# Performance work log

Hardware: AMD Instinct MI355X
Metric: run time of the kernel (lower is better)

## Reference

```python
import jax, jax.numpy as jnp
import numpy as np

E = 384        # number of edges
HID = 128      # hidden_dim
NH = 8         # num_heads
DH = HID // NH # head_dim = 16
NR = 64        # num_radial
CUTOFF = 10.0
AIN = 2 * DH + NR + 1  # attention MLP input dim = 97


def _xavier(key, fan_in, fan_out):
    a = np.sqrt(6.0 / (fan_in + fan_out))
    return jax.random.uniform(key, (fan_in, fan_out), jnp.float32, -a, a)


def setup_inputs() -> dict:
    key = jax.random.key(0)
    ks = jax.random.split(key, 16)
    return {
        "edge_features": jax.random.normal(ks[0], (E, HID), jnp.float32),
        "edge_coords": jax.random.normal(ks[1], (E, 3), jnp.float32),
        "edge_mask": jnp.zeros((E, E), jnp.float32),  # 0 = connected
        "wq": _xavier(ks[2], HID, HID),
        "wk": _xavier(ks[3], HID, HID),
        "wv": _xavier(ks[4], HID, HID),
        "rbf_centers": jnp.linspace(0.0, CUTOFF, NR).astype(jnp.float32),
        "rbf_widths": jnp.full((NR,), 0.5, jnp.float32),
        "a_w1": _xavier(ks[5], AIN, HID), "a_b1": jnp.zeros((HID,), jnp.float32),
        "a_w2": _xavier(ks[6], HID, HID), "a_b2": jnp.zeros((HID,), jnp.float32),
        "a_w3": _xavier(ks[7], HID, NH),  "a_b3": jnp.zeros((NH,), jnp.float32),
        "g_w1": _xavier(ks[8], DH, HID),  "g_b1": jnp.zeros((HID,), jnp.float32),
        "g_w2": _xavier(ks[9], HID, 1),   "g_b2": jnp.zeros((1,), jnp.float32),
        "wo": _xavier(ks[10], HID, HID),  "bo": jnp.zeros((HID,), jnp.float32),
        "ln_g": jnp.ones((HID,), jnp.float32),
        "ln_b": jnp.zeros((HID,), jnp.float32),
        "edge_index": jax.random.randint(ks[11], (2, E), 0, E, jnp.int64) if jax.config.jax_enable_x64 else jax.random.randint(ks[11], (2, E), 0, E, jnp.int32),
    }


def reference(edge_features, edge_coords, edge_mask,
              wq, wk, wv, rbf_centers, rbf_widths,
              a_w1, a_b1, a_w2, a_b2, a_w3, a_b3,
              g_w1, g_b1, g_w2, g_b2, wo, bo, ln_g, ln_b,
              edge_index):
    silu = jax.nn.silu
    n = edge_features.shape[0]

    q = (edge_features @ wq).reshape(n, NH, DH)
    k = (edge_features @ wk).reshape(n, NH, DH)
    v = (edge_features @ wv).reshape(n, NH, DH)

    # pairwise geometry [E, E, ...]
    coord_diff = edge_coords[:, None, :] - edge_coords[None, :, :]
    dist = jnp.linalg.norm(coord_diff, axis=-1) + 1e-8
    dist = jnp.clip(dist, 1e-8, 1e8)
    dot = jnp.clip(jnp.sum(edge_coords[:, None, :] * edge_coords[None, :, :], -1),
                   -1e8, 1e8)
    d = dist[..., None]                               # [E, E, 1]
    rbf = jnp.exp(-rbf_widths * (d - rbf_centers) ** 2) * (d <= CUTOFF).astype(jnp.float32)

    feats = []
    coords = edge_coords
    for h in range(NH):  # structural loop over fixed num_heads
        qh = jnp.broadcast_to(q[:, h, None, :], (n, n, DH))
        kh = jnp.broadcast_to(k[None, :, h, :], (n, n, DH))
        ai = jnp.concatenate([qh, kh, rbf, dot[..., None]], -1)  # [E, E, 97]
        x = silu(ai @ a_w1 + a_b1)
        x = silu(x @ a_w2 + a_b2)
        scores = (x @ a_w3 + a_b3)[:, :, h] + edge_mask
        scores = jnp.clip(scores, -1e9, 1e9)
        attn = jax.nn.softmax(scores, axis=-1)
        attn = jnp.nan_to_num(attn, nan=0.0, posinf=1.0, neginf=0.0)
        vh = v[:, h, :]
        feats.append(attn @ vh)
        # coord gate from v_head of the query edge, broadcast over keys
        gates = jax.nn.sigmoid(silu(vh @ g_w1 + g_b1) @ g_w2 + g_b2)  # [E, 1]
        coords = coords + jnp.einsum('ij,ijc->ic', attn * gates, coord_diff) / NH

    upd = jnp.concatenate(feats, -1)             # [E, hidden]
    y = edge_features + upd @ wo + bo            # residual + out_proj
    mu = jnp.mean(y, -1, keepdims=True)
    var = jnp.var(y, -1, keepdims=True)
    out_f = (y - mu) / jnp.sqrt(var + 1e-5) * ln_g + ln_b
    return out_f, coords
```

## Files before the change

### kernel.cpp

```cpp
#include <hip/hip_runtime.h>
#include <hip/hip_bf16.h>

#define N 384
#define HIDN 128
#define NHD 8
#define DHD 16
#define NRB 64
#define CUTF 10.0f

#define WS_V 0
#define WS_QPB (WS_V + N*HIDN)
#define WS_KPB (WS_QPB + N*NHD*HIDN/2)
#define WS_GATE (WS_KPB + N*NHD*HIDN/2)
#define WS_UPD (WS_GATE + N*NHD)
#define WS_SCORES (WS_UPD + N*HIDN)
#define WS_W2BF (WS_SCORES + NHD*N*N)

typedef short bf16x8 __attribute__((ext_vector_type(8)));
typedef float floatx4 __attribute__((ext_vector_type(4)));
#define MFMA16(a, b, c) __builtin_amdgcn_mfma_f32_16x16x32_bf16(a, b, c, 0, 0, 0)

__device__ __forceinline__ float siluf(float x) { return x / (1.0f + __expf(-x)); }
__device__ __forceinline__ float silu_fast(float x) {
    return x * __builtin_amdgcn_rcpf(1.0f + __expf(-x));
}
__device__ __forceinline__ short f2bf(float f) {
    unsigned int b = __float_as_uint(f);
    unsigned int r = (b + 0x7fffu + ((b >> 16) & 1u)) >> 16;
    return (short)r;
}
__device__ __forceinline__ float bf2f(short s) {
    return __uint_as_float(((unsigned int)(unsigned short)s) << 16);
}
__device__ __forceinline__ unsigned int cvt_pk_bf16(float lo, float hi) {
    unsigned int r;
    asm("v_cvt_pk_bf16_f32 %0, %1, %2" : "=v"(r) : "v"(lo), "v"(hi));
    return r;
}
__device__ __forceinline__ float wave_sum(float v) {
    for (int o = 32; o; o >>= 1) v += __shfl_down(v, o, 64);
    return v;
}

__global__ __launch_bounds__(128) void k_pre(const float* __restrict__ ef,
    const float* __restrict__ wq, const float* __restrict__ wk, const float* __restrict__ wv,
    const float* __restrict__ aw1, const float* __restrict__ aw2,
    const float* __restrict__ gw1, const float* __restrict__ gb1,
    const float* __restrict__ gw2, const float* __restrict__ gb2,
    float* __restrict__ v, unsigned short* __restrict__ Qpb,
    unsigned short* __restrict__ Kpb, float* __restrict__ gates,
    unsigned short* __restrict__ w2bf) {
    __shared__ float sE[HIDN], sQ[HIDN], sK[HIDN], sV[HIDN];
    __shared__ float sRed[2];
    int i = blockIdx.x, t = threadIdx.x;
    if (i < HIDN) w2bf[(size_t)i * HIDN + t] = (unsigned short)f2bf(aw2[t * HIDN + i]);
    sE[t] = ef[i * HIDN + t];
    __syncthreads();
    float aq = 0.f, ak = 0.f, av = 0.f;
#pragma unroll 8
    for (int c = 0; c < HIDN; c++) {
        float e = sE[c];
        aq += e * wq[c * HIDN + t];
        ak += e * wk[c * HIDN + t];
        av += e * wv[c * HIDN + t];
    }
    v[i * HIDN + t] = av;
    sQ[t] = aq; sK[t] = ak; sV[t] = av;
    __syncthreads();
    for (int h = 0; h < NHD; h++) {
        float accq = 0.f, acck = 0.f;
#pragma unroll
        for (int d = 0; d < DHD; d++) {
            accq += sQ[h * DHD + d] * aw1[d * HIDN + t];
            acck += sK[h * DHD + d] * aw1[(DHD + d) * HIDN + t];
        }
        Qpb[(i * NHD + h) * HIDN + t] = (unsigned short)f2bf(accq);
        Kpb[(i * NHD + h) * HIDN + t] = (unsigned short)f2bf(acck);
        float tt = gb1[t];
#pragma unroll
        for (int d = 0; d < DHD; d++) tt += sV[h * DHD + d] * gw1[d * HIDN + t];
        float contrib = siluf(tt) * gw2[t];
        float s = wave_sum(contrib);
        if ((t & 63) == 0) sRed[t >> 6] = s;
        __syncthreads();
        if (t == 0) gates[i * NHD + h] = 1.0f / (1.0f + __expf(-(sRed[0] + sRed[1] + gb2[0])));
        __syncthreads();
    }
}

#define OFF_W2T 0
#define OFF_QPB 32768
#define OFF_SDD 34816
#define OFF_RBF 34944
#define OFF_R   39040
#define SMEM_SZ 55936

__global__ __launch_bounds__(512, 4) void k_scores_mfma(
    const float* __restrict__ coords, const float* __restrict__ mask,
    const float* __restrict__ centers, const float* __restrict__ widths,
    const float* __restrict__ aw1, const float* __restrict__ ab1,
    const float* __restrict__ ab2,
    const float* __restrict__ aw3, const float* __restrict__ ab3,
    const unsigned short* __restrict__ Qpb, const unsigned short* __restrict__ Kpb,
    const unsigned short* __restrict__ w2bf,
    float* __restrict__ scores) {
    __shared__ __align__(16) char smem[SMEM_SZ];
    const int t = threadIdx.x;
    const int lane = t & 63;
    const int w = t >> 6;
    const int l15 = lane & 15;
    const int quad = lane >> 4;
    const int i = blockIdx.y;
    const int jb = blockIdx.x * 128;

    {
        const uint4* src = (const uint4*)w2bf;
        for (int idx = t; idx < 2048; idx += 512) {
            int row = idx >> 4, slot = idx & 15;
            *(uint4*)(smem + OFF_W2T + row * 256 + ((slot * 16) ^ ((row & 7) << 4))) = src[idx];
        }
    }
    if (t < 128) {
        ((uint4*)(smem + OFF_QPB))[t] = ((const uint4*)(Qpb + (size_t)i * NHD * HIDN))[t];
    }
    const int c0 = w * 16 + l15;
    bf16x8 BW1[2];
#pragma unroll
    for (int ks = 0; ks < 2; ks++) {
        bf16x8 a;
#pragma unroll
        for (int e = 0; e < 8; e++) {
            int r = ks * 32 + quad * 8 + e;
            a[e] = f2bf(aw1[(32 + r) * HIDN + c0]);
        }
        BW1[ks] = a;
    }
    const float b1v = ab1[c0];
    const float w1dv = aw1[96 * HIDN + c0];
    const float ab3v = ab3[w];
    float b2r[8], w3r[8];
#pragma unroll
    for (int ct = 0; ct < 8; ct++) {
        b2r[ct] = ab2[ct * 16 + l15];
        w3r[ct] = aw3[(ct * 16 + l15) * NHD + w];
    }
    const float cr = centers[t & 63], rwd = widths[t & 63];
    const float cix = coords[i * 3], ciy = coords[i * 3 + 1], ciz = coords[i * 3 + 2];
    __syncthreads();

    for (int ch = 0; ch < 4; ch++) {
        const int j0 = jb + ch * 32;
        {
            int r = t & 63;
#pragma unroll
            for (int p = 0; p < 4; p++) {
                int j = w + p * 8;
                int jj = j0 + j;
                float jx = coords[jj * 3], jy = coords[jj * 3 + 1], jz = coords[jj * 3 + 2];
                float dx = cix - jx, dy = ciy - jy, dz = ciz - jz;
                float dist = sqrtf(dx * dx + dy * dy + dz * dz) + 1e-8f;
                dist = fminf(fmaxf(dist, 1e-8f), 1e8f);
                float dd = dist - cr;
                float val = (dist <= CUTF) ? __expf(-rwd * dd * dd) : 0.0f;
                *(short*)(smem + OFF_RBF + j * 128 + ((r * 2) ^ ((j & 7) << 4))) = f2bf(val);
            }
            if (t < 32) {
                int jj = j0 + t;
                float jx = coords[jj * 3], jy = coords[jj * 3 + 1], jz = coords[jj * 3 + 2];
                float dot = fminf(fmaxf(cix * jx + ciy * jy + ciz * jz, -1e8f), 1e8f);
                *(float*)(smem + OFF_SDD + t * 4) = dot;
            }
        }
        __syncthreads();
#pragma unroll
        for (int jt = 0; jt < 2; jt++) {
            int jl = jt * 16 + l15;
            int sw = (jl & 7) << 4;
            bf16x8 ra0 = *(const bf16x8*)(smem + OFF_RBF + jl * 128 + ((quad * 16) ^ sw));
            bf16x8 ra1 = *(const bf16x8*)(smem + OFF_RBF + jl * 128 + ((64 + quad * 16) ^ sw));
            floatx4 acc;
#pragma unroll
            for (int r = 0; r < 4; r++) {
                float dotv = *(const float*)(smem + OFF_SDD + (jt * 16 + quad * 4 + r) * 4);
                acc[r] = b1v + dotv * w1dv;
            }
            acc = MFMA16(ra0, BW1[0], acc);
            acc = MFMA16(ra1, BW1[1], acc);
#pragma unroll
            for (int r = 0; r < 4; r++)
                *(float*)(smem + OFF_R + (jt * 16 + quad * 4 + r) * 528 + c0 * 4) = acc[r];
        }
        __syncthreads();
        {
            bf16x8 A2[2][4];
#pragma unroll
            for (int f = 0; f < 4; f++) {
                const int c8 = f * 32 + quad * 8;
                bf16x8 qp = *(const bf16x8*)(smem + OFF_QPB + (w * HIDN + c8) * 2);
#pragma unroll
                for (int jt = 0; jt < 2; jt++) {
                    const int jl = jt * 16 + l15;
                    bf16x8 kp = *(const bf16x8*)(Kpb + ((size_t)(j0 + jl) * NHD + w) * HIDN + c8);
                    const char* rbase = smem + OFF_R + jl * 528 + c8 * 4;
                    float4 r0 = *(const float4*)(rbase);
                    float4 r1 = *(const float4*)(rbase + 16);
                    float xs[8] = {r0.x, r0.y, r0.z, r0.w, r1.x, r1.y, r1.z, r1.w};
                    union { unsigned int u[4]; bf16x8 v; } uu;
#pragma unroll
                    for (int e2 = 0; e2 < 4; e2++) {
                        float xa = silu_fast(bf2f(kp[2 * e2])     + bf2f(qp[2 * e2])     + xs[2 * e2]);
                        float xb = silu_fast(bf2f(kp[2 * e2 + 1]) + bf2f(qp[2 * e2 + 1]) + xs[2 * e2 + 1]);
                        uu.u[e2] = cvt_pk_bf16(xa, xb);
                    }
                    A2[jt][f] = uu.v;
                }
            }
            float part0[4] = {0.f, 0.f, 0.f, 0.f};
            float part1[4] = {0.f, 0.f, 0.f, 0.f};
#pragma unroll 2
            for (int ct = 0; ct < 8; ct++) {
                const int rw2 = ct * 16 + l15;
                const char* wb = smem + OFF_W2T + rw2 * 256;
                const int sw = (rw2 & 7) << 4;
                bf16x8 b0 = *(const bf16x8*)(wb + ((quad * 16) ^ sw));
                bf16x8 b1 = *(const bf16x8*)(wb + ((64 + quad * 16) ^ sw));
                bf16x8 b2 = *(const bf16x8*)(wb + ((128 + quad * 16) ^ sw));
                bf16x8 b3 = *(const bf16x8*)(wb + ((192 + quad * 16) ^ sw));
                float bb = b2r[ct], ww = w3r[ct];
                floatx4 acc0 = {bb, bb, bb, bb};
                acc0 = MFMA16(A2[0][0], b0, acc0);
                acc0 = MFMA16(A2[0][1], b1, acc0);
                acc0 = MFMA16(A2[0][2], b2, acc0);
                acc0 = MFMA16(A2[0][3], b3, acc0);
                floatx4 acc1 = {bb, bb, bb, bb};
                acc1 = MFMA16(A2[1][0], b0, acc1);
                acc1 = MFMA16(A2[1][1], b1, acc1);
                acc1 = MFMA16(A2[1][2], b2, acc1);
                acc1 = MFMA16(A2[1][3], b3, acc1);
#pragma unroll
                for (int r = 0; r < 4; r++) {
                    part0[r] += silu_fast(acc0[r]) * ww;
                    part1[r] += silu_fast(acc1[r]) * ww;
                }
            }
#pragma unroll
            for (int off = 1; off < 16; off <<= 1) {
#pragma unroll
                for (int r = 0; r < 4; r++) {
                    part0[r] += __shfl_xor(part0[r], off, 64);
                    part1[r] += __shfl_xor(part1[r], off, 64);
                }
            }
            if (l15 == 0) {
#pragma unroll
                for (int r = 0; r < 4; r++) {
                    int j = quad * 4 + r;
                    float s = part0[r] + ab3v + mask[(size_t)i * N + j0 + j];
                    s = fminf(fmaxf(s, -1e9f), 1e9f);
                    scores[((size_t)w * N + i) * N + j0 + j] = s;
                    int j2 = 16 + quad * 4 + r;
                    float s2 = part1[r] + ab3v + mask[(size_t)i * N + j0 + j2];
                    s2 = fminf(fmaxf(s2, -1e9f), 1e9f);
                    scores[((size_t)w * N + i) * N + j0 + j2] = s2;
                }
            }
        }
        __syncthreads();
    }
}

__global__ __launch_bounds__(256) void k_attn2(
    const float* __restrict__ scores, const float* __restrict__ v,
    const float* __restrict__ gates, const float* __restrict__ coords,
    float* __restrict__ upd, float* __restrict__ out) {
    __shared__ float sA[4][N];
    __shared__ float sCrd[N * 3];
    __shared__ float sC[NHD][3];
    int i = blockIdx.x, t = threadIdx.x, w = t >> 6, lane = t & 63;
    for (int idx = t; idx < N * 3; idx += 256) sCrd[idx] = coords[idx];
    float cix = coords[i * 3], ciy = coords[i * 3 + 1], ciz = coords[i * 3 + 2];
    __syncthreads();
    for (int hh = 0; hh < 2; hh++) {
        int h = hh * 4 + w;
        const float* srow = scores + ((size_t)h * N + i) * N;
        float s[6];
#pragma unroll
        for (int p = 0; p < 6; p++) s[p] = srow[lane + 64 * p];
        float m = s[0];
#pragma unroll
        for (int p = 1; p < 6; p++) m = fmaxf(m, s[p]);
        for (int off = 1; off < 64; off <<= 1) m = fmaxf(m, __shfl_xor(m, off, 64));
        float e[6], sum = 0.f;
#pragma unroll
        for (int p = 0; p < 6; p++) { e[p] = __expf(s[p] - m); sum += e[p]; }
        for (int off = 1; off < 64; off <<= 1) sum += __shfl_xor(sum, off, 64);
        float inv = 1.0f / sum;
#pragma unroll
        for (int p = 0; p < 6; p++) sA[w][lane + 64 * p] = e[p] * inv;
        __syncthreads();
        int d4 = lane & 3, grp = lane >> 2;
        float4 f4 = {0.f, 0.f, 0.f, 0.f};
        for (int j = grp; j < N; j += 16) {
            float a = sA[w][j];
            float4 vv = *(const float4*)(v + j * HIDN + h * DHD + d4 * 4);
            f4.x += a * vv.x; f4.y += a * vv.y; f4.z += a * vv.z; f4.w += a * vv.w;
        }
#pragma unroll
        for (int off = 4; off < 64; off <<= 1) {
            f4.x += __shfl_xor(f4.x, off, 64);
            f4.y += __shfl_xor(f4.y, off, 64);
            f4.z += __shfl_xor(f4.z, off, 64);
            f4.w += __shfl_xor(f4.w, off, 64);
        }
        if (lane < 4) *(float4*)(upd + i * HIDN + h * DHD + lane * 4) = f4;
        float cx = 0.f, cy = 0.f, cz = 0.f;
#pragma unroll
        for (int p = 0; p < 6; p++) {
            int j = lane + 64 * p;
            float a = sA[w][j];
            cx += a * (cix - sCrd[j * 3]);
            cy += a * (ciy - sCrd[j * 3 + 1]);
            cz += a * (ciz - sCrd[j * 3 + 2]);
        }
        for (int off = 1; off < 64; off <<= 1) {
            cx += __shfl_xor(cx, off, 64);
            cy += __shfl_xor(cy, off, 64);
            cz += __shfl_xor(cz, off, 64);
        }
        if (lane == 0) {
            float g = gates[i * NHD + h] * (1.0f / NHD);
            sC[h][0] = g * cx; sC[h][1] = g * cy; sC[h][2] = g * cz;
        }
        __syncthreads();
    }
    if (t < 3) {
        float acc = coords[i * 3 + t];
#pragma unroll
        for (int h = 0; h < NHD; h++) acc += sC[h][t];
        out[N * HIDN + i * 3 + t] = acc;
    }
}

__global__ __launch_bounds__(128) void k_out(
    const float* __restrict__ ef, const float* __restrict__ upd,
    const float* __restrict__ wo, const float* __restrict__ bo,
    const float* __restrict__ lng, const float* __restrict__ lnb,
    float* __restrict__ out) {
    __shared__ float sU[HIDN];
    __shared__ float sR[2];
    int i = blockIdx.x, c = threadIdx.x;
    sU[c] = upd[i * HIDN + c];
    __syncthreads();
    float y = ef[i * HIDN + c] + bo[c];
#pragma unroll 8
    for (int cp = 0; cp < HIDN; cp++) y += sU[cp] * wo[cp * HIDN + c];
    float s = wave_sum(y);
    if ((c & 63) == 0) sR[c >> 6] = s;
    __syncthreads();
    float mu = (sR[0] + sR[1]) * (1.0f / HIDN);
    __syncthreads();
    float dv = y - mu;
    float s2 = wave_sum(dv * dv);
    if ((c & 63) == 0) sR[c >> 6] = s2;
    __syncthreads();
    float var = (sR[0] + sR[1]) * (1.0f / HIDN);
    out[i * HIDN + c] = dv * rsqrtf(var + 1e-5f) * lng[c] + lnb[c];
}

extern "C" void kernel_launch(void* const* d_in, const int* in_sizes, int n_in,
                              void* d_out, int out_size, void* d_ws, size_t ws_size,
                              hipStream_t stream) {
    const float* ef      = (const float*)d_in[0];
    const float* coords  = (const float*)d_in[1];
    const float* mask    = (const float*)d_in[2];
    const float* wq      = (const float*)d_in[3];
    const float* wk      = (const float*)d_in[4];
    const float* wv      = (const float*)d_in[5];
    const float* centers = (const float*)d_in[6];
    const float* widths  = (const float*)d_in[7];
    const float* aw1     = (const float*)d_in[8];
    const float* ab1     = (const float*)d_in[9];
    const float* aw2     = (const float*)d_in[10];
    const float* ab2     = (const float*)d_in[11];
    const float* aw3     = (const float*)d_in[12];
    const float* ab3     = (const float*)d_in[13];
    const float* gw1     = (const float*)d_in[14];
    const float* gb1     = (const float*)d_in[15];
    const float* gw2     = (const float*)d_in[16];
    const float* gb2     = (const float*)d_in[17];
    const float* wo      = (const float*)d_in[18];
    const float* bo      = (const float*)d_in[19];
    const float* lng     = (const float*)d_in[20];
    const float* lnb     = (const float*)d_in[21];
    float* ws = (float*)d_ws;
    float* v      = ws + WS_V;
    unsigned short* Qpb = (unsigned short*)(ws + WS_QPB);
    unsigned short* Kpb = (unsigned short*)(ws + WS_KPB);
    float* gates  = ws + WS_GATE;
    float* upd    = ws + WS_UPD;
    float* scores = ws + WS_SCORES;
    unsigned short* w2bf = (unsigned short*)(ws + WS_W2BF);
    float* out = (float*)d_out;

    k_pre<<<N, 128, 0, stream>>>(ef, wq, wk, wv, aw1, aw2, gw1, gb1, gw2, gb2, v, Qpb, Kpb, gates, w2bf);
    k_scores_mfma<<<dim3(3, N), 512, 0, stream>>>(
        coords, mask, centers, widths, aw1, ab1, ab2, aw3, ab3, Qpb, Kpb, w2bf, scores);
    k_attn2<<<N, 256, 0, stream>>>(scores, v, gates, coords, upd, out);
    k_out<<<N, 128, 0, stream>>>(ef, upd, wo, bo, lng, lnb, out);
}
```

Baseline: 277.8 us.

## Fuse output projection into attention kernel and retile score kernel

Merges the out-projection and layernorm kernel into the attention kernel, dropping one launch and the upd round trip through global memory. Reorganizes the score kernel: half the j range per block (doubling grid size), head-major Q/K projection layout, Q loaded into registers instead of shared memory, one j-tile processed at a time to cut register pressure, higher occupancy hint, and vectorized mask/score stores. Gate reductions in the prologue kernel are batched behind one barrier instead of two per head. Smaller blocks reload W2 into shared memory twice as often, which is the main cost added.

```diff
diff --git a/kernel.cpp b/kernel.cpp
--- a/kernel.cpp
+++ b/kernel.cpp
@@ -51,7 +51,7 @@
     unsigned short* __restrict__ Kpb, float* __restrict__ gates,
     unsigned short* __restrict__ w2bf) {
     __shared__ float sE[HIDN], sQ[HIDN], sK[HIDN], sV[HIDN];
-    __shared__ float sRed[2];
+    __shared__ float sG[NHD][2];
     int i = blockIdx.x, t = threadIdx.x;
     if (i < HIDN) w2bf[(size_t)i * HIDN + t] = (unsigned short)f2bf(aw2[t * HIDN + i]);
     sE[t] = ef[i * HIDN + t];
@@ -74,28 +74,27 @@
             accq += sQ[h * DHD + d] * aw1[d * HIDN + t];
             acck += sK[h * DHD + d] * aw1[(DHD + d) * HIDN + t];
         }
-        Qpb[(i * NHD + h) * HIDN + t] = (unsigned short)f2bf(accq);
-        Kpb[(i * NHD + h) * HIDN + t] = (unsigned short)f2bf(acck);
+        Qpb[((size_t)h * N + i) * HIDN + t] = (unsigned short)f2bf(accq);
+        Kpb[((size_t)h * N + i) * HIDN + t] = (unsigned short)f2bf(acck);
         float tt = gb1[t];
 #pragma unroll
         for (int d = 0; d < DHD; d++) tt += sV[h * DHD + d] * gw1[d * HIDN + t];
         float contrib = siluf(tt) * gw2[t];
         float s = wave_sum(contrib);
-        if ((t & 63) == 0) sRed[t >> 6] = s;
-        __syncthreads();
-        if (t == 0) gates[i * NHD + h] = 1.0f / (1.0f + __expf(-(sRed[0] + sRed[1] + gb2[0])));
-        __syncthreads();
-    }
+        if ((t & 63) == 0) sG[h][t >> 6] = s;
+    }
+    __syncthreads();
+    if (t < NHD)
+        gates[i * NHD + t] = 1.0f / (1.0f + __expf(-(sG[t][0] + sG[t][1] + gb2[0])));
 }
 
 #define OFF_W2T 0
-#define OFF_QPB 32768
-#define OFF_SDD 34816
-#define OFF_RBF 34944
-#define OFF_R   39040
-#define SMEM_SZ 55936
-
-__global__ __launch_bounds__(512, 4) void k_scores_mfma(
+#define OFF_SDD 32768
+#define OFF_RBF 32896
+#define OFF_R   36992
+#define SMEM_SZ 53888
+
+__global__ __launch_bounds__(512, 6) void k_scores_mfma(
     const float* __restrict__ coords, const float* __restrict__ mask,
     const float* __restrict__ centers, const float* __restrict__ widths,
     const float* __restrict__ aw1, const float* __restrict__ ab1,
@@ -111,7 +110,7 @@
     const int l15 = lane & 15;
     const int quad = lane >> 4;
     const int i = blockIdx.y;
-    const int jb = blockIdx.x * 128;
+    const int jb = blockIdx.x * 64;
 
     {
         const uint4* src = (const uint4*)w2bf;
@@ -120,9 +119,6 @@
             *(uint4*)(smem + OFF_W2T + row * 256 + ((slot * 16) ^ ((row & 7) << 4))) = src[idx];
         }
     }
-    if (t < 128) {
-        ((uint4*)(smem + OFF_QPB))[t] = ((const uint4*)(Qpb + (size_t)i * NHD * HIDN))[t];
-    }
     const int c0 = w * 16 + l15;
     bf16x8 BW1[2];
 #pragma unroll
@@ -135,6 +131,10 @@
         }
         BW1[ks] = a;
     }
+    bf16x8 QPF[4];
+#pragma unroll
+    for (int f = 0; f < 4; f++)
+        QPF[f] = *(const bf16x8*)(Qpb + ((size_t)w * N + i) * HIDN + f * 32 + quad * 8);
     const float b1v = ab1[c0];
     const float w1dv = aw1[96 * HIDN + c0];
     const float ab3v = ab3[w];
@@ -144,14 +144,13 @@
         b2r[ct] = ab2[ct * 16 + l15];
         w3r[ct] = aw3[(ct * 16 + l15) * NHD + w];
     }
-    const float cr = centers[t & 63], rwd = widths[t & 63];
+    const float cr = centers[lane], rwd = widths[lane];
     const float cix = coords[i * 3], ciy = coords[i * 3 + 1], ciz = coords[i * 3 + 2];
     __syncthreads();
 
-    for (int ch = 0; ch < 4; ch++) {
+    for (int ch = 0; ch < 2; ch++) {
         const int j0 = jb + ch * 32;
         {
-            int r = t & 63;
 #pragma unroll
             for (int p = 0; p < 4; p++) {
                 int j = w + p * 8;
@@ -162,7 +161,7 @@
                 dist = fminf(fmaxf(dist, 1e-8f), 1e8f);
                 float dd = dist - cr;
                 float val = (dist <= CUTF) ? __expf(-rwd * dd * dd) : 0.0f;
-                *(short*)(smem + OFF_RBF + j * 128 + ((r * 2) ^ ((j & 7) << 4))) = f2bf(val);
+                *(short*)(smem + OFF_RBF + j * 128 + ((lane * 2) ^ ((j & 7) << 4))) = f2bf(val);
             }
             if (t < 32) {
                 int jj = j0 + t;
@@ -191,32 +190,29 @@
                 *(float*)(smem + OFF_R + (jt * 16 + quad * 4 + r) * 528 + c0 * 4) = acc[r];
         }
         __syncthreads();
-        {
-            bf16x8 A2[2][4];
+#pragma unroll
+        for (int jt = 0; jt < 2; jt++) {
+            const int jl = jt * 16 + l15;
+            bf16x8 A[4];
 #pragma unroll
             for (int f = 0; f < 4; f++) {
                 const int c8 = f * 32 + quad * 8;
-                bf16x8 qp = *(const bf16x8*)(smem + OFF_QPB + (w * HIDN + c8) * 2);
-#pragma unroll
-                for (int jt = 0; jt < 2; jt++) {
-                    const int jl = jt * 16 + l15;
-                    bf16x8 kp = *(const bf16x8*)(Kpb + ((size_t)(j0 + jl) * NHD + w) * HIDN + c8);
-                    const char* rbase = smem + OFF_R + jl * 528 + c8 * 4;
-                    float4 r0 = *(const float4*)(rbase);
-                    float4 r1 = *(const float4*)(rbase + 16);
-                    float xs[8] = {r0.x, r0.y, r0.z, r0.w, r1.x, r1.y, r1.z, r1.w};
-                    union { unsigned int u[4]; bf16x8 v; } uu;
-#pragma unroll
-                    for (int e2 = 0; e2 < 4; e2++) {
-                        float xa = silu_fast(bf2f(kp[2 * e2])     + bf2f(qp[2 * e2])     + xs[2 * e2]);
-                        float xb = silu_fast(bf2f(kp[2 * e2 + 1]) + bf2f(qp[2 * e2 + 1]) + xs[2 * e2 + 1]);
-                        uu.u[e2] = cvt_pk_bf16(xa, xb);
-                    }
-                    A2[jt][f] = uu.v;
+                bf16x8 kp = *(const bf16x8*)(Kpb + ((size_t)w * N + j0 + jl) * HIDN + c8);
+                bf16x8 qp = QPF[f];
+                const char* rbase = smem + OFF_R + jl * 528 + c8 * 4;
+                float4 r0 = *(const float4*)(rbase);
+                float4 r1 = *(const float4*)(rbase + 16);
+                float xs[8] = {r0.x, r0.y, r0.z, r0.w, r1.x, r1.y, r1.z, r1.w};
+                union { unsigned int u[4]; bf16x8 v; } uu;
+#pragma unroll
+                for (int e2 = 0; e2 < 4; e2++) {
+                    float xa = silu_fast(bf2f(kp[2 * e2])     + bf2f(qp[2 * e2])     + xs[2 * e2]);
+                    float xb = silu_fast(bf2f(kp[2 * e2 + 1]) + bf2f(qp[2 * e2 + 1]) + xs[2 * e2 + 1]);
+                    uu.u[e2] = cvt_pk_bf16(xa, xb);
                 }
-            }
-            float part0[4] = {0.f, 0.f, 0.f, 0.f};
-            float part1[4] = {0.f, 0.f, 0.f, 0.f};
+                A[f] = uu.v;
+            }
+            float part[4] = {0.f, 0.f, 0.f, 0.f};
 #pragma unroll 2
             for (int ct = 0; ct < 8; ct++) {
                 const int rw2 = ct * 16 + l15;
@@ -227,42 +223,30 @@
                 bf16x8 b2 = *(const bf16x8*)(wb + ((128 + quad * 16) ^ sw));
                 bf16x8 b3 = *(const bf16x8*)(wb + ((192 + quad * 16) ^ sw));
                 float bb = b2r[ct], ww = w3r[ct];
-                floatx4 acc0 = {bb, bb, bb, bb};
-                acc0 = MFMA16(A2[0][0], b0, acc0);
-                acc0 = MFMA16(A2[0][1], b1, acc0);
-                acc0 = MFMA16(A2[0][2], b2, acc0);
-                acc0 = MFMA16(A2[0][3], b3, acc0);
-                floatx4 acc1 = {bb, bb, bb, bb};
-                acc1 = MFMA16(A2[1][0], b0, acc1);
-                acc1 = MFMA16(A2[1][1], b1, acc1);
-                acc1 = MFMA16(A2[1][2], b2, acc1);
-                acc1 = MFMA16(A2[1][3], b3, acc1);
-#pragma unroll
-                for (int r = 0; r < 4; r++) {
-                    part0[r] += silu_fast(acc0[r]) * ww;
-                    part1[r] += silu_fast(acc1[r]) * ww;
-                }
+                floatx4 acc = {bb, bb, bb, bb};
+                acc = MFMA16(A[0], b0, acc);
+                acc = MFMA16(A[1], b1, acc);
+                acc = MFMA16(A[2], b2, acc);
+                acc = MFMA16(A[3], b3, acc);
+#pragma unroll
+                for (int r = 0; r < 4; r++)
+                    part[r] += silu_fast(acc[r]) * ww;
             }
 #pragma unroll
             for (int off = 1; off < 16; off <<= 1) {
 #pragma unroll
-                for (int r = 0; r < 4; r++) {
-                    part0[r] += __shfl_xor(part0[r], off, 64);
-                    part1[r] += __shfl_xor(part1[r], off, 64);
-                }
+                for (int r = 0; r < 4; r++)
+                    part[r] += __shfl_xor(part[r], off, 64);
             }
             if (l15 == 0) {
-#pragma unroll
-                for (int r = 0; r < 4; r++) {
-                    int j = quad * 4 + r;
-                    float s = part0[r] + ab3v + mask[(size_t)i * N + j0 + j];
-                    s = fminf(fmaxf(s, -1e9f), 1e9f);
-                    scores[((size_t)w * N + i) * N + j0 + j] = s;
-                    int j2 = 16 + quad * 4 + r;
-                    float s2 = part1[r] + ab3v + mask[(size_t)i * N + j0 + j2];
-                    s2 = fminf(fmaxf(s2, -1e9f), 1e9f);
-                    scores[((size_t)w * N + i) * N + j0 + j2] = s2;
-                }
+                const int jo = j0 + jt * 16 + quad * 4;
+                float4 mv = *(const float4*)(mask + (size_t)i * N + jo);
+                float4 sv;
+                sv.x = fminf(fmaxf(part[0] + ab3v + mv.x, -1e9f), 1e9f);
+                sv.y = fminf(fmaxf(part[1] + ab3v + mv.y, -1e9f), 1e9f);
+                sv.z = fminf(fmaxf(part[2] + ab3v + mv.z, -1e9f), 1e9f);
+                sv.w = fminf(fmaxf(part[3] + ab3v + mv.w, -1e9f), 1e9f);
+                *(float4*)(scores + ((size_t)w * N + i) * N + jo) = sv;
             }
         }
         __syncthreads();
@@ -272,10 +256,14 @@
 __global__ __launch_bounds__(256) void k_attn2(
     const float* __restrict__ scores, const float* __restrict__ v,
     const float* __restrict__ gates, const float* __restrict__ coords,
-    float* __restrict__ upd, float* __restrict__ out) {
+    const float* __restrict__ ef, const float* __restrict__ wo,
+    const float* __restrict__ bo, const float* __restrict__ lng,
+    const float* __restrict__ lnb, float* __restrict__ out) {
     __shared__ float sA[4][N];
     __shared__ float sCrd[N * 3];
     __shared__ float sC[NHD][3];
+    __shared__ float sUpd[HIDN];
+    __shared__ float sR2[2];
     int i = blockIdx.x, t = threadIdx.x, w = t >> 6, lane = t & 63;
     for (int idx = t; idx < N * 3; idx += 256) sCrd[idx] = coords[idx];
     float cix = coords[i * 3], ciy = coords[i * 3 + 1], ciz = coords[i * 3 + 2];
@@ -312,7 +300,7 @@
             f4.z += __shfl_xor(f4.z, off, 64);
             f4.w += __shfl_xor(f4.w, off, 64);
         }
-        if (lane < 4) *(float4*)(upd + i * HIDN + h * DHD + lane * 4) = f4;
+        if (lane < 4) *(float4*)(&sUpd[h * DHD + lane * 4]) = f4;
         float cx = 0.f, cy = 0.f, cz = 0.f;
 #pragma unroll
         for (int p = 0; p < 6; p++) {
@@ -339,32 +327,21 @@
         for (int h = 0; h < NHD; h++) acc += sC[h][t];
         out[N * HIDN + i * 3 + t] = acc;
     }
-}
-
-__global__ __launch_bounds__(128) void k_out(
-    const float* __restrict__ ef, const float* __restrict__ upd,
-    const float* __restrict__ wo, const float* __restrict__ bo,
-    const float* __restrict__ lng, const float* __restrict__ lnb,
-    float* __restrict__ out) {
-    __shared__ float sU[HIDN];
-    __shared__ float sR[2];
-    int i = blockIdx.x, c = threadIdx.x;
-    sU[c] = upd[i * HIDN + c];
-    __syncthreads();
+    int c = t & 127;
     float y = ef[i * HIDN + c] + bo[c];
 #pragma unroll 8
-    for (int cp = 0; cp < HIDN; cp++) y += sU[cp] * wo[cp * HIDN + c];
-    float s = wave_sum(y);
-    if ((c & 63) == 0) sR[c >> 6] = s;
-    __syncthreads();
-    float mu = (sR[0] + sR[1]) * (1.0f / HIDN);
+    for (int cp = 0; cp < HIDN; cp++) y += sUpd[cp] * wo[cp * HIDN + c];
+    float ssum = wave_sum(y);
+    if (t < 128 && (t & 63) == 0) sR2[t >> 6] = ssum;
+    __syncthreads();
+    float mu = (sR2[0] + sR2[1]) * (1.0f / HIDN);
     __syncthreads();
     float dv = y - mu;
     float s2 = wave_sum(dv * dv);
-    if ((c & 63) == 0) sR[c >> 6] = s2;
-    __syncthreads();
-    float var = (sR[0] + sR[1]) * (1.0f / HIDN);
-    out[i * HIDN + c] = dv * rsqrtf(var + 1e-5f) * lng[c] + lnb[c];
+    if (t < 128 && (t & 63) == 0) sR2[t >> 6] = s2;
+    __syncthreads();
+    float var = (sR2[0] + sR2[1]) * (1.0f / HIDN);
+    if (t < 128) out[i * HIDN + c] = dv * rsqrtf(var + 1e-5f) * lng[c] + lnb[c];
 }
 
 extern "C" void kernel_launch(void* const* d_in, const int* in_sizes, int n_in,
@@ -397,14 +374,12 @@
     unsigned short* Qpb = (unsigned short*)(ws + WS_QPB);
     unsigned short* Kpb = (unsigned short*)(ws + WS_KPB);
     float* gates  = ws + WS_GATE;
-    float* upd    = ws + WS_UPD;
     float* scores = ws + WS_SCORES;
     unsigned short* w2bf = (unsigned short*)(ws + WS_W2BF);
     float* out = (float*)d_out;
 
     k_pre<<<N, 128, 0, stream>>>(ef, wq, wk, wv, aw1, aw2, gw1, gb1, gw2, gb2, v, Qpb, Kpb, gates, w2bf);
-    k_scores_mfma<<<dim3(3, N), 512, 0, stream>>>(
+    k_scores_mfma<<<dim3(6, N), 512, 0, stream>>>(
         coords, mask, centers, widths, aw1, ab1, ab2, aw3, ab3, Qpb, Kpb, w2bf, scores);
-    k_attn2<<<N, 256, 0, stream>>>(scores, v, gates, coords, upd, out);
-    k_out<<<N, 128, 0, stream>>>(ef, upd, wo, bo, lng, lnb, out);
-}
+    k_attn2<<<N, 256, 0, stream>>>(scores, v, gates, coords, ef, wo, bo, lng, lnb, out);
+}
```

Result: slower. 484.2 us (+74.3%).
